# Kernel tuning notes

Hardware: AMD Instinct MI355X
Metric: run time of the kernel (lower is better)

The kernel has to match this reference:

```python
import jax, jax.numpy as jnp
import numpy as np

N = 1024          # number of nodes
E = 32768         # number of edges
S = 4             # num_scales
STEPS = 31        # num_steps
MIN_SIGMA = 0.1
MAX_SIGMA = 3.0
EPS = 1e-12       # F.normalize eps


def setup_inputs() -> dict:
    key = jax.random.key(0)
    k1, k2 = jax.random.split(key, 2)
    coords = jax.random.normal(k1, (N, 3), dtype=jnp.float32)
    edge_index = jax.random.randint(k2, (2, E), 0, N, dtype=jnp.int64)
    # learned parameter, initialized exactly as in the module
    log_sigmas = jnp.linspace(jnp.log(jnp.float32(MIN_SIGMA)),
                              jnp.log(jnp.float32(MAX_SIGMA)), S).astype(jnp.float32)
    return {"coords": coords, "log_sigmas": log_sigmas, "edge_index": edge_index}


def reference(coords, log_sigmas, edge_index):
    n = coords.shape[0]
    # pairwise squared euclidean distances (cdist(..)^2)  [N,N]
    diff = coords[:, None, :] - coords[None, :, :]
    d2 = jnp.sum(diff * diff, axis=-1)

    sigmas = jnp.sort(jnp.exp(log_sigmas))                       # [S]
    w = jnp.exp(-d2[None, :, :] / (2.0 * sigmas[:, None, None] ** 2))  # [S,N,N]
    eye = jnp.eye(n, dtype=w.dtype)
    w = w * (1.0 - eye)                                          # zero diagonal
    row_sum = jnp.sum(w, axis=2, keepdims=True)                  # L1 row norm (w>=0)
    P = w / jnp.maximum(row_sum, EPS)                            # row-stochastic, 0 rows -> 0

    ei, ej = edge_index[0], edge_index[1]

    def step(P_k, _):
        P_k = P_k @ P                                            # batched [S,N,N] GEMM
        diag = jnp.diagonal(P_k, axis1=1, axis2=2)               # [S,N]
        edge = P_k[:, ei, ej]                                    # [S,E]
        return P_k, (diag, edge)

    P0 = jnp.broadcast_to(eye, P.shape)
    _, (diags, edges) = jax.lax.scan(step, P0, None, length=STEPS)
    # diags: [STEPS,S,N] -> node features [N, S*STEPS] (scale-major, step-minor)
    node_features = jnp.transpose(diags, (2, 1, 0)).reshape(n, S * STEPS)
    edge_features = jnp.transpose(edges, (2, 1, 0)).reshape(ei.shape[0], S * STEPS)
    return node_features, edge_features
```

## Files before the change

### kernel.cpp

```cpp
#include <hip/hip_runtime.h>

#define N 1024
#define NE 32768
#define S 4
#define STEPS 31
#define FEAT (S * STEPS)
#define PLANE ((size_t)S * N * N)
#define MAXT 192

typedef short short8 __attribute__((ext_vector_type(8)));
typedef short short4v __attribute__((ext_vector_type(4)));
typedef float f32x4 __attribute__((ext_vector_type(4)));

__device__ __forceinline__ ushort f2bf(float x) {
    union { float f; unsigned u; } v; v.f = x;
    unsigned r = v.u + 0x7fffu + ((v.u >> 16) & 1u);
    return (ushort)(r >> 16);
}
__device__ __forceinline__ float bf2f(ushort h) {
    union { unsigned u; float f; } v; v.u = ((unsigned)h) << 16;
    return v.f;
}

__device__ __forceinline__ void gload16(const ushort* g, ushort* l) {
    __builtin_amdgcn_global_load_lds(
        (const __attribute__((address_space(1))) unsigned int*)g,
        (__attribute__((address_space(3))) unsigned int*)l, 16, 0, 0);
}

__global__ __launch_bounds__(256) void build_P(const float* __restrict__ coords,
                                               const float* __restrict__ log_sigmas,
                                               ushort* __restrict__ Oh,
                                               ushort* __restrict__ Ol)
{
    const int i   = blockIdx.x;
    const int tid = threadIdx.x;

    float sg[S];
#pragma unroll
    for (int s = 0; s < S; ++s) sg[s] = expf(log_sigmas[s]);
#define CSWP(a, b) { float lo = fminf(sg[a], sg[b]); float hi = fmaxf(sg[a], sg[b]); sg[a] = lo; sg[b] = hi; }
    CSWP(0, 1) CSWP(2, 3) CSWP(0, 2) CSWP(1, 3) CSWP(1, 2)
#undef CSWP
    float inv2s2[S];
#pragma unroll
    for (int s = 0; s < S; ++s) inv2s2[s] = 1.0f / (2.0f * sg[s] * sg[s]);

    const float cx = coords[3 * i + 0];
    const float cy = coords[3 * i + 1];
    const float cz = coords[3 * i + 2];

    float w[4][S];
    float part[S] = {0.f, 0.f, 0.f, 0.f};
#pragma unroll
    for (int c = 0; c < 4; ++c) {
        const int j = tid + c * 256;
        const float dx = cx - coords[3 * j + 0];
        const float dy = cy - coords[3 * j + 1];
        const float dz = cz - coords[3 * j + 2];
        const float d2 = dx * dx + dy * dy + dz * dz;
#pragma unroll
        for (int s = 0; s < S; ++s) {
            const float v = (j == i) ? 0.0f : expf(-d2 * inv2s2[s]);
            w[c][s] = v;
            part[s] += v;
        }
    }

    __shared__ float red[S][256];
#pragma unroll
    for (int s = 0; s < S; ++s) red[s][tid] = part[s];
    __syncthreads();
    for (int st = 128; st > 0; st >>= 1) {
        if (tid < st) {
#pragma unroll
            for (int s = 0; s < S; ++s) red[s][tid] += red[s][tid + st];
        }
        __syncthreads();
    }

    float invden[S];
#pragma unroll
    for (int s = 0; s < S; ++s) invden[s] = 1.0f / fmaxf(red[s][0], 1e-12f);

#pragma unroll
    for (int c = 0; c < 4; ++c) {
        const int j = tid + c * 256;
#pragma unroll
        for (int s = 0; s < S; ++s) {
            const float p = w[c][s] * invden[s];
            const size_t off = ((size_t)s * N + i) * N + j;
            const ushort h = f2bf(p);
            Oh[off] = h;
            Ol[off] = f2bf(p - bf2f(h));
        }
    }
}

__global__ __launch_bounds__(256) void transpose_hl(const ushort* __restrict__ Xh,
                                                    const ushort* __restrict__ Xl,
                                                    ushort* __restrict__ Yh,
                                                    ushort* __restrict__ Yl)
{
    __shared__ float tile[64][65];
    const size_t zb = (size_t)blockIdx.z * N * N;
    const int tr = blockIdx.y * 64, tc = blockIdx.x * 64;
    const int tid = threadIdx.x;
    const int c  = tid & 63;
    const int r0 = tid >> 6;
#pragma unroll
    for (int i = 0; i < 16; ++i) {
        const int r = r0 + i * 4;
        const size_t idx = zb + (size_t)(tr + r) * N + tc + c;
        tile[r][c] = bf2f(Xh[idx]) + bf2f(Xl[idx]);
    }
    __syncthreads();
#pragma unroll
    for (int i = 0; i < 16; ++i) {
        const int r = r0 + i * 4;
        const size_t idx = zb + (size_t)(tc + r) * N + tr + c;
        const float x = tile[c][r];
        const ushort h = f2bf(x);
        Yh[idx] = h;
        if (Yl) Yl[idx] = f2bf(x - bf2f(h));
    }
}

template <bool SPLIT>
__device__ __forceinline__ void gemm_body(const ushort* __restrict__ Ah,
                                          const ushort* __restrict__ Al,
                                          const ushort* __restrict__ BTh,
                                          const ushort* __restrict__ BTl,
                                          ushort* __restrict__ Ch,
                                          ushort* __restrict__ Cl,
                                          ushort* __restrict__ CTh,
                                          ushort* __restrict__ CTl,
                                          int id)
{
    constexpr int NP = SPLIT ? 4 : 2;
    __shared__ ushort smem[4][NP][128 * 32];
    const int tid  = threadIdx.x;
    const int w    = tid >> 6;
    const int lane = tid & 63;
    const int wr   = w >> 1;
    const int wc   = w & 1;

    const int yrow = id & 7;
    const int rest = id >> 3;
    const int xcol = rest & 7;
    const int z    = rest >> 3;
    const size_t zb = (size_t)z * N * N;
    const int tr = yrow * 128;
    const int tc = xcol * 128;

    const ushort* gA0 = Ah  + zb + (size_t)tr * N;
    const ushort* gA1 = SPLIT ? (Al  + zb + (size_t)tr * N) : nullptr;
    const ushort* gB0 = BTh + zb + (size_t)tc * N;
    const ushort* gB1 = SPLIT ? (BTl + zb + (size_t)tc * N) : nullptr;

    f32x4 acc[2][4] = {};

    auto STAGE = [&](int bufi, int k0) __attribute__((always_inline)) {
        const int row = tid >> 2;
        const int kg  = (tid & 3) ^ ((row >> 1) & 3);
        const size_t go = (size_t)row * N + k0 + kg * 8;
        const int lb = w * 512;
        gload16(gA0 + go, &smem[bufi][0][lb]);
        if constexpr (SPLIT) {
            gload16(gA1 + go, &smem[bufi][1][lb]);
            gload16(gB0 + go, &smem[bufi][2][lb]);
            gload16(gB1 + go, &smem[bufi][3][lb]);
        } else {
            gload16(gB0 + go, &smem[bufi][1][lb]);
        }
    };

    const int lrow = lane & 15;
    const int lkg  = lane >> 4;

    auto COMPUTE = [&](int bufi) __attribute__((always_inline)) {
        short8 ah[2], al[2], bh[4], bl[4];
#pragma unroll
        for (int m = 0; m < 2; ++m) {
            const int arow = wr * 32 + m * 16 + lrow;
            const int aoff = arow * 32 + ((lkg ^ ((arow >> 1) & 3)) << 3);
            ah[m] = *(const short8*)&smem[bufi][0][aoff];
            if constexpr (SPLIT) al[m] = *(const short8*)&smem[bufi][1][aoff];
        }
#pragma unroll
        for (int n = 0; n < 4; ++n) {
            const int brow = wc * 64 + n * 16 + lrow;
            const int boff = brow * 32 + ((lkg ^ ((brow >> 1) & 3)) << 3);
            if constexpr (SPLIT) {
                bh[n] = *(const short8*)&smem[bufi][2][boff];
                bl[n] = *(const short8*)&smem[bufi][3][boff];
            } else {
                bh[n] = *(const short8*)&smem[bufi][1][boff];
            }
        }
        __builtin_amdgcn_s_setprio(1);
#pragma unroll
        for (int m = 0; m < 2; ++m)
#pragma unroll
            for (int n = 0; n < 4; ++n) {
                acc[m][n] = __builtin_amdgcn_mfma_f32_16x16x32_bf16(ah[m], bh[n], acc[m][n], 0, 0, 0);
                if constexpr (SPLIT) {
                    acc[m][n] = __builtin_amdgcn_mfma_f32_16x16x32_bf16(ah[m], bl[n], acc[m][n], 0, 0, 0);
                    acc[m][n] = __builtin_amdgcn_mfma_f32_16x16x32_bf16(al[m], bh[n], acc[m][n], 0, 0, 0);
                }
            }
        __builtin_amdgcn_s_setprio(0);
    };

    STAGE(0, 0);
    STAGE(1, 32);
#pragma unroll 1
    for (int t = 0; t < 32; ++t) {
        __builtin_amdgcn_sched_barrier(0);
        if (t < 30) {
            STAGE((t + 2) & 3, (t + 2) * 32);
            if constexpr (SPLIT) asm volatile("s_waitcnt vmcnt(8)" ::: "memory");
            else                 asm volatile("s_waitcnt vmcnt(4)" ::: "memory");
        } else if (t == 30) {
            if constexpr (SPLIT) asm volatile("s_waitcnt vmcnt(4)" ::: "memory");
            else                 asm volatile("s_waitcnt vmcnt(2)" ::: "memory");
        } else {
            asm volatile("s_waitcnt vmcnt(0)" ::: "memory");
        }
        __builtin_amdgcn_s_barrier();
        __builtin_amdgcn_sched_barrier(0);
        COMPUTE(t & 3);
        __builtin_amdgcn_sched_barrier(0);
    }

#pragma unroll
    for (int m = 0; m < 2; ++m)
#pragma unroll
    for (int n = 0; n < 4; ++n) {
        const f32x4 v = acc[m][n];
        ushort hs[4], ls[4];
#pragma unroll
        for (int r = 0; r < 4; ++r) {
            const float x = v[r];
            hs[r] = f2bf(x);
            ls[r] = f2bf(x - bf2f(hs[r]));
        }
        const int row0 = tr + wr * 32 + m * 16 + lkg * 4;
        const int col  = tc + wc * 64 + n * 16 + lrow;
        if (Ch) {
#pragma unroll
            for (int r = 0; r < 4; ++r) {
                const size_t idx = zb + (size_t)(row0 + r) * N + col;
                Ch[idx] = hs[r];
                if (Cl) Cl[idx] = ls[r];
            }
        }
        if (CTh) {
            short4v hv;
            hv[0] = (short)hs[0]; hv[1] = (short)hs[1];
            hv[2] = (short)hs[2]; hv[3] = (short)hs[3];
            *(short4v*)&CTh[zb + (size_t)col * N + row0] = hv;
            if (CTl) {
                short4v lv;
                lv[0] = (short)ls[0]; lv[1] = (short)ls[1];
                lv[2] = (short)ls[2]; lv[3] = (short)ls[3];
                *(short4v*)&CTl[zb + (size_t)col * N + row0] = lv;
            }
        }
    }
}

template <bool SPLIT>
__global__ __launch_bounds__(512) void gemm_tile(const ushort* __restrict__ Ah,
                                                 const ushort* __restrict__ Al,
                                                 const ushort* __restrict__ BTh,
                                                 const ushort* __restrict__ BTl,
                                                 ushort* __restrict__ Ch,
                                                 ushort* __restrict__ Cl,
                                                 ushort* __restrict__ CTh,
                                                 ushort* __restrict__ CTl)
{
    gemm_body<SPLIT>(Ah, Al, BTh, BTl, Ch, Cl, CTh, CTl, blockIdx.x);
}

__global__ __launch_bounds__(512) void gemm_leaf(
    const ushort* A0, const ushort* B0, ushort* C0, ushort* T0,
    const ushort* A1, const ushort* B1, ushort* C1, ushort* T1,
    const ushort* A2, const ushort* B2, ushort* C2, ushort* T2,
    const ushort* A3, const ushort* B3, ushort* C3, ushort* T3)
{
    const int op = blockIdx.x >> 8;
    const int id = blockIdx.x & 255;
    const ushort* A; const ushort* B; ushort* C; ushort* T;
    if      (op == 0) { A = A0; B = B0; C = C0; T = T0; }
    else if (op == 1) { A = A1; B = B1; C = C1; T = T1; }
    else if (op == 2) { A = A2; B = B2; C = C2; T = T2; }
    else              { A = A3; B = B3; C = C3; T = T3; }
    gemm_body<false>(A, nullptr, B, nullptr, C, nullptr, T, nullptr, id);
}

__global__ __launch_bounds__(256) void gather_hl(const ushort* __restrict__ Ph,
                                                 const ushort* __restrict__ Pl,
                                                 const int* __restrict__ eidx,
                                                 float* __restrict__ out,
                                                 int t)
{
    const int tid = blockIdx.x * blockDim.x + threadIdx.x;
    const int ND = S * N;
    if (tid < ND) {
        const int s = tid >> 10;
        const int n = tid & (N - 1);
        const size_t off = ((size_t)s * N + n) * N + n;
        float v = bf2f(Ph[off]);
        if (Pl) v += bf2f(Pl[off]);
        out[(size_t)n * FEAT + s * STEPS + t] = v;
    } else {
        const int idx = tid - ND;
        if (idx >= S * NE) return;
        const int s = idx >> 15;
        const int e = idx & (NE - 1);
        const int i = eidx[e];
        const int j = eidx[NE + e];
        const size_t off = ((size_t)s * N + i) * N + j;
        float v = bf2f(Ph[off]);
        if (Pl) v += bf2f(Pl[off]);
        out[(size_t)N * FEAT + (size_t)e * FEAT + s * STEPS + t] = v;
    }
}

__global__ __launch_bounds__(256) void zero_aux(int* __restrict__ p, int n)
{
    for (int i = blockIdx.x * 256 + threadIdx.x; i < n; i += gridDim.x * 256) p[i] = 0;
}

__global__ __launch_bounds__(256) void edge_hist(const int* __restrict__ eidx,
                                                 int* __restrict__ hist)
{
    const int e = blockIdx.x * 256 + threadIdx.x;
    if (e < NE) atomicAdd(&hist[eidx[NE + e]], 1);
}

__global__ __launch_bounds__(1024) void scan1024(const int* __restrict__ hist,
                                                 int* __restrict__ offs)
{
    __shared__ int tmp[1024];
    const int t = threadIdx.x;
    tmp[t] = hist[t];
    __syncthreads();
    for (int d = 1; d < 1024; d <<= 1) {
        int v = (t >= d) ? tmp[t - d] : 0;
        __syncthreads();
        tmp[t] += v;
        __syncthreads();
    }
    offs[t + 1] = tmp[t];
    if (t == 0) offs[0] = 0;
}

__global__ __launch_bounds__(256) void edge_scatter(const int* __restrict__ eidx,
                                                    const int* __restrict__ offs,
                                                    int* __restrict__ cursor,
                                                    int* __restrict__ perm)
{
    const int e = blockIdx.x * 256 + threadIdx.x;
    if (e < NE) {
        const int j = eidx[NE + e];
        const int pos = atomicAdd(&cursor[j], 1);
        perm[offs[j] + pos] = e;
    }
}

__global__ __launch_bounds__(256) void extract_k(const ushort* __restrict__ BT18,
                                                 const ushort* __restrict__ bt9,
                                                 const ushort* __restrict__ bt10,
                                                 const ushort* __restrict__ bt11,
                                                 const ushort* __restrict__ bt12,
                                                 const ushort* __restrict__ A12,
                                                 const ushort* __restrict__ A24,
                                                 const int* __restrict__ eidx,
                                                 const int* __restrict__ perm,
                                                 const int* __restrict__ offs,
                                                 float* __restrict__ out)
{
    const int id = blockIdx.x;
    const int s  = (id & 7) >> 1;
    const int j  = (id >> 3) * 2 + (id & 1);
    const int tid  = threadIdx.x;
    const int wave = tid >> 6;
    const int lane = tid & 63;

    __shared__ __align__(16) ushort bt[12][1032];
    __shared__ int tlist[MAXT];
    __shared__ int elist[MAXT];

    const int base  = offs[j];
    const int cnt   = min(offs[j + 1] - base, MAXT - 1);
    const int ntask = cnt + 1;
    const int ngrp  = (ntask + 15) >> 4;

    for (int t0 = tid; t0 < MAXT; t0 += 256) {
        int e = -2, i = j;
        if (t0 < cnt)       { e = perm[base + t0]; i = eidx[e]; }
        else if (t0 == cnt) { e = -1; }
        tlist[t0] = i;
        elist[t0] = e;
    }

    const size_t rowbase = ((size_t)s * N + j) * N;
#pragma unroll
    for (int bb = 0; bb < 6; ++bb) {
        const int b0 = 2 * bb, b1 = 2 * bb + 1;
        const ushort* q0 = (b0 < 8) ? (BT18 + (size_t)b0 * PLANE)
                                    : (b0 == 8 ? bt9 : b0 == 9 ? bt10 : b0 == 10 ? bt11 : bt12);
        const ushort* q1 = (b1 < 8) ? (BT18 + (size_t)b1 * PLANE)
                                    : (b1 == 8 ? bt9 : b1 == 9 ? bt10 : b1 == 10 ? bt11 : bt12);
        const ushort* q  = (tid < 128) ? q0 : q1;
        const int b  = b0 + (tid >> 7);
        const int ch = tid & 127;
        const short8 v = *(const short8*)&q[rowbase + ch * 8];
        *(short8*)&bt[b][ch * 8] = v;
    }
    __syncthreads();

    for (int t0 = tid; t0 < ntask; t0 += 256) {
        const int i = tlist[t0];
        const int e = elist[t0];
        const size_t obase = (e >= 0)
            ? ((size_t)N * FEAT + (size_t)e * FEAT + (size_t)s * STEPS)
            : ((size_t)j * FEAT + (size_t)s * STEPS);
#pragma unroll
        for (int b = 0; b < 12; ++b)
            out[obase + b] = bf2f(bt[b][i]);
    }

    const int nidx = lane & 15;
    const ushort* bt_ptr = &bt[nidx < 12 ? nidx : 0][(lane >> 4) * 8];

    for (int g = wave; g < ngrp; g += 4) {
        const int i = tlist[g * 16 + nidx];
        const size_t abase = ((size_t)s * N + i) * N + ((lane >> 4) * 8);
        const ushort* pa0 = A12 + abase;
        const ushort* pa1 = A24 + abase;

        f32x4 acc0 = {}, acc1 = {};
#pragma unroll 4
        for (int ks = 0; ks < 32; ++ks) {
            const short8 bf  = *(const short8*)(bt_ptr + ks * 32);
            const short8 af0 = *(const short8*)(pa0 + ks * 32);
            const short8 af1 = *(const short8*)(pa1 + ks * 32);
            acc0 = __builtin_amdgcn_mfma_f32_16x16x32_bf16(af0, bf, acc0, 0, 0, 0);
            acc1 = __builtin_amdgcn_mfma_f32_16x16x32_bf16(af1, bf, acc1, 0, 0, 0);
        }

        if (nidx < 12) {
            const int m0 = (lane >> 4) * 4;
#pragma unroll
            for (int r = 0; r < 4; ++r) {
                const int e = elist[g * 16 + m0 + r];
                if (e >= -1) {
                    const size_t obase = (e >= 0)
                        ? ((size_t)N * FEAT + (size_t)e * FEAT + (size_t)s * STEPS)
                        : ((size_t)j * FEAT + (size_t)s * STEPS);
                    out[obase + 12 + nidx] = acc0[r];
                    if (nidx < 7)
                        out[obase + 24 + nidx] = acc1[r];
                }
            }
        }
    }
}

extern "C" void kernel_launch(void* const* d_in, const int* in_sizes, int n_in,
                              void* d_out, int out_size, void* d_ws, size_t ws_size,
                              hipStream_t stream)
{
    const float* coords     = (const float*)d_in[0];
    const float* log_sigmas = (const float*)d_in[1];
    const int*   eidx       = (const int*)d_in[2];
    float*       out        = (float*)d_out;

    ushort* W = (ushort*)d_ws;
    const dim3 tgrid(16, 16, S);
    ushort* const NUL = nullptr;
#define PS(k) (W + (size_t)(k) * PLANE)

    const size_t AUX_INTS = 1024 + 1024 + 1025 + NE;
    const size_t NEED_A   = 15 * PLANE * sizeof(ushort) + AUX_INTS * sizeof(int);

    if (ws_size >= NEED_A) {
        int* hist   = (int*)(W + 15 * PLANE);
        int* cursor = hist + 1024;
        int* offs   = cursor + 1024;
        int* perm   = offs + 1025;

        zero_aux<<<8, 256, 0, stream>>>(hist, 2048);
        edge_hist<<<NE / 256, 256, 0, stream>>>(eidx, hist);
        scan1024<<<1, 1024, 0, stream>>>(hist, offs);
        edge_scatter<<<NE / 256, 256, 0, stream>>>(eidx, offs, cursor, perm);

        build_P<<<N, 256, 0, stream>>>(coords, log_sigmas, PS(8), PS(9));
        transpose_hl<<<tgrid, 256, 0, stream>>>(PS(8), PS(9), PS(0), PS(10));

        gemm_tile<true><<<256, 512, 0, stream>>>(PS(8), PS(9), PS(0), PS(10),
                                                 PS(12), PS(13), PS(1), PS(11));
        gemm_tile<true><<<256, 512, 0, stream>>>(PS(12), PS(13), PS(1), PS(11),
                                                 PS(14), PS(8), PS(3), NUL);
        gemm_tile<true><<<256, 512, 0, stream>>>(PS(14), PS(8), PS(1), PS(11),
                                                 PS(13), PS(9), PS(5), NUL);
        gemm_tile<true><<<256, 512, 0, stream>>>(PS(13), PS(9), PS(1), PS(11),
                                                 PS(8), NUL, PS(7), NUL);
        gemm_leaf<<<768, 512, 0, stream>>>(
            PS(12), PS(0), NUL, PS(2),
            PS(14), PS(0), NUL, PS(4),
            PS(13), PS(0), NUL, PS(6),
            NUL, NUL, NUL, NUL);
        gemm_leaf<<<1024, 512, 0, stream>>>(
            PS(8), PS(0), NUL, PS(13),
            PS(8), PS(1), NUL, PS(14),
            PS(8), PS(2), NUL, PS(10),
            PS(8), PS(3), PS(12), PS(11));
        gemm_tile<false><<<256, 512, 0, stream>>>(PS(12), NUL, PS(11), NUL,
                                                  PS(9), NUL, NUL, NUL);

        extract_k<<<N * S, 256, 0, stream>>>(PS(0), PS(13), PS(14), PS(10), PS(11),
                                             PS(12), PS(9), eidx, perm, offs, out);
    } else {
        ushort* ping_h = PS(0); ushort* ping_l = PS(1);
        ushort* pong_h = PS(2); ushort* pong_l = PS(3);
        ushort* bt_h   = PS(4); ushort* bt_l   = PS(5);
        const int gather_blocks = (S * N + S * NE + 255) / 256;

        build_P<<<N, 256, 0, stream>>>(coords, log_sigmas, ping_h, ping_l);
        gather_hl<<<gather_blocks, 256, 0, stream>>>(ping_h, ping_l, eidx, out, 0);
        transpose_hl<<<tgrid, 256, 0, stream>>>(ping_h, ping_l, bt_h, bt_l);

        ushort* cur_h = ping_h; ushort* cur_l = ping_l;
        ushort* nxt_h = pong_h; ushort* nxt_l = pong_l;
        for (int k = 2; k <= STEPS; ++k) {
            gemm_tile<true><<<256, 512, 0, stream>>>(cur_h, cur_l, bt_h, bt_l,
                                                     nxt_h, nxt_l, NUL, NUL);
            gather_hl<<<gather_blocks, 256, 0, stream>>>(nxt_h, nxt_l, eidx, out, k - 1);
            ushort* th = cur_h; ushort* tl = cur_l;
            cur_h = nxt_h; cur_l = nxt_l; nxt_h = th; nxt_l = tl;
        }
    }
#undef PS
}
```

Before: 356.1 us.

## Restructure power-chain schedule to compute fewer split-precision GEMMs

New measurement: 347.1 us. 1.03x faster.

```diff
diff --git a/kernel.cpp b/kernel.cpp
--- a/kernel.cpp
+++ b/kernel.cpp
@@ -370,11 +370,7 @@
     }
 }
 
-__global__ __launch_bounds__(256) void extract_k(const ushort* __restrict__ BT18,
-                                                 const ushort* __restrict__ bt9,
-                                                 const ushort* __restrict__ bt10,
-                                                 const ushort* __restrict__ bt11,
-                                                 const ushort* __restrict__ bt12,
+__global__ __launch_bounds__(256) void extract_k(const ushort* __restrict__ BT,
                                                  const ushort* __restrict__ A12,
                                                  const ushort* __restrict__ A24,
                                                  const int* __restrict__ eidx,
@@ -407,17 +403,10 @@
     }
 
     const size_t rowbase = ((size_t)s * N + j) * N;
-#pragma unroll
-    for (int bb = 0; bb < 6; ++bb) {
-        const int b0 = 2 * bb, b1 = 2 * bb + 1;
-        const ushort* q0 = (b0 < 8) ? (BT18 + (size_t)b0 * PLANE)
-                                    : (b0 == 8 ? bt9 : b0 == 9 ? bt10 : b0 == 10 ? bt11 : bt12);
-        const ushort* q1 = (b1 < 8) ? (BT18 + (size_t)b1 * PLANE)
-                                    : (b1 == 8 ? bt9 : b1 == 9 ? bt10 : b1 == 10 ? bt11 : bt12);
-        const ushort* q  = (tid < 128) ? q0 : q1;
-        const int b  = b0 + (tid >> 7);
-        const int ch = tid & 127;
-        const short8 v = *(const short8*)&q[rowbase + ch * 8];
+    for (int c = tid; c < 12 * 128; c += 256) {
+        const int b  = c >> 7;
+        const int ch = c & 127;
+        const short8 v = *(const short8*)&BT[(size_t)b * PLANE + rowbase + ch * 8];
         *(short8*)&bt[b][ch * 8] = v;
     }
     __syncthreads();
@@ -434,11 +423,12 @@
     }
 
     const int nidx = lane & 15;
-    const ushort* bt_ptr = &bt[nidx < 12 ? nidx : 0][(lane >> 4) * 8];
+    const int koff = (lane >> 4) * 8;
+    const ushort* bt_ptr = &bt[nidx < 12 ? nidx : 0][koff];
 
     for (int g = wave; g < ngrp; g += 4) {
         const int i = tlist[g * 16 + nidx];
-        const size_t abase = ((size_t)s * N + i) * N + ((lane >> 4) * 8);
+        const size_t abase = ((size_t)s * N + i) * N + koff;
         const ushort* pa0 = A12 + abase;
         const ushort* pa1 = A24 + abase;
 
@@ -498,32 +488,31 @@
         scan1024<<<1, 1024, 0, stream>>>(hist, offs);
         edge_scatter<<<NE / 256, 256, 0, stream>>>(eidx, offs, cursor, perm);
 
-        build_P<<<N, 256, 0, stream>>>(coords, log_sigmas, PS(8), PS(9));
-        transpose_hl<<<tgrid, 256, 0, stream>>>(PS(8), PS(9), PS(0), PS(10));
-
-        gemm_tile<true><<<256, 512, 0, stream>>>(PS(8), PS(9), PS(0), PS(10),
-                                                 PS(12), PS(13), PS(1), PS(11));
-        gemm_tile<true><<<256, 512, 0, stream>>>(PS(12), PS(13), PS(1), PS(11),
-                                                 PS(14), PS(8), PS(3), NUL);
-        gemm_tile<true><<<256, 512, 0, stream>>>(PS(14), PS(8), PS(1), PS(11),
-                                                 PS(13), PS(9), PS(5), NUL);
-        gemm_tile<true><<<256, 512, 0, stream>>>(PS(13), PS(9), PS(1), PS(11),
-                                                 PS(8), NUL, PS(7), NUL);
+        build_P<<<N, 256, 0, stream>>>(coords, log_sigmas, PS(12), PS(13));
+        transpose_hl<<<tgrid, 256, 0, stream>>>(PS(12), PS(13), PS(0), PS(4));
+
+        gemm_tile<true><<<256, 512, 0, stream>>>(PS(12), PS(13), PS(0), PS(4),
+                                                 PS(6), PS(10), PS(1), PS(5));
+        gemm_tile<true><<<256, 512, 0, stream>>>(PS(6), PS(10), PS(1), PS(5),
+                                                 PS(11), PS(8), PS(3), PS(9));
         gemm_leaf<<<768, 512, 0, stream>>>(
-            PS(12), PS(0), NUL, PS(2),
-            PS(14), PS(0), NUL, PS(4),
-            PS(13), PS(0), NUL, PS(6),
+            PS(6), PS(0), NUL, PS(2),
+            PS(11), PS(0), NUL, PS(4),
+            PS(11), PS(1), NUL, PS(5),
             NUL, NUL, NUL, NUL);
+        gemm_tile<true><<<256, 512, 0, stream>>>(PS(11), PS(8), PS(3), PS(9),
+                                                 PS(12), NUL, PS(7), NUL);
         gemm_leaf<<<1024, 512, 0, stream>>>(
-            PS(8), PS(0), NUL, PS(13),
-            PS(8), PS(1), NUL, PS(14),
-            PS(8), PS(2), NUL, PS(10),
-            PS(8), PS(3), PS(12), PS(11));
-        gemm_tile<false><<<256, 512, 0, stream>>>(PS(12), NUL, PS(11), NUL,
-                                                  PS(9), NUL, NUL, NUL);
-
-        extract_k<<<N * S, 256, 0, stream>>>(PS(0), PS(13), PS(14), PS(10), PS(11),
-                                             PS(12), PS(9), eidx, perm, offs, out);
+            PS(11), PS(2), NUL, PS(6),
+            PS(12), PS(0), NUL, PS(8),
+            PS(12), PS(1), NUL, PS(9),
+            PS(12), PS(2), NUL, PS(10));
+        gemm_tile<false><<<256, 512, 0, stream>>>(PS(12), NUL, PS(3), NUL,
+                                                  PS(13), NUL, PS(11), NUL);
+        gemm_tile<false><<<256, 512, 0, stream>>>(PS(13), NUL, PS(11), NUL,
+                                                  PS(14), NUL, NUL, NUL);
+
+        extract_k<<<N * S, 256, 0, stream>>>(W, PS(13), PS(14), eidx, perm, offs, out);
     } else {
         ushort* ping_h = PS(0); ushort* ping_l = PS(1);
         ushort* pong_h = PS(2); ushort* pong_l = PS(3);
```
